# Kernel optimization log

Hardware: AMD Instinct MI355X
Metric: run time of the kernel (lower is better)

Reference implementation:

```python
import jax, jax.numpy as jnp
import numpy as np

# Stochastic-computing layer: values in [0,1] are encoded as random bitstreams
# (bit = uniform <= value), multiply = AND, and the reduction over input rows is
# a chained random MUX (tf.where with p=0.5 coins), then mean over the bit axis.
BATCH, D_IN, D_OUT, BIT_SIZE = 512, 1024, 1024, 128


def setup_inputs() -> dict:
    key = jax.random.key(0)
    kx, kw = jax.random.split(key)
    # bitstream-encoded probabilities in [0, 1]
    x = jax.random.uniform(kx, (BATCH, D_IN), dtype=jnp.float32)
    w = jax.random.uniform(kw, (D_IN, D_OUT), dtype=jnp.float32)
    return {"x": x, "w": w}


def reference(x, w):
    B, Din = x.shape
    Dout = w.shape[1]
    key = jax.random.key(42)
    kx, kw, kc = jax.random.split(key, 3)

    # bitstream generation: bit = (uniform <= value)
    x_bits = jax.random.uniform(kx, (B, Din, BIT_SIZE)) <= x[:, :, None]        # (B, Din, T) bool
    w_bits = jax.random.uniform(kw, (Din, Dout, BIT_SIZE)) <= w[:, :, None]     # (Din, Dout, T) bool

    # Chained random MUX over rows 1..Din-2 (mirrors `for row in range(1, dim-1)`):
    #   final = where(coin, final, row_r)  ->  result is row r of the LAST step
    #   whose coin was False; row 0 if every coin was True. Coins are shared
    #   across the output dim (original select_line shape (B, 1, T)).
    n_steps = Din - 2
    coins = jax.random.uniform(kc, (n_steps, B, BIT_SIZE)) <= 0.5               # (steps, B, T) bool
    rows = jnp.arange(1, Din - 1)                                               # (steps,)
    idx = jnp.max(jnp.where(~coins, rows[:, None, None], 0), axis=0)            # (B, T) int

    # Gather the selected row's bits instead of materializing (B, Din, Dout, T)
    chosen_x = jnp.take_along_axis(x_bits, idx[:, None, :], axis=1)[:, 0, :]    # (B, T)
    w_bt = jnp.transpose(w_bits, (0, 2, 1))                                     # (Din, T, Dout)
    chosen_w = w_bt[idx, jnp.arange(BIT_SIZE)[None, :], :]                      # (B, T, Dout)

    # stochastic multiply (AND) then decode via mean over the bit axis
    final = (chosen_x[:, :, None] & chosen_w).astype(jnp.float32)               # (B, T, Dout)
    return jnp.mean(final, axis=1)                                              # (B, Dout)
```

## Files before the change

kernel.cpp:

```cpp
#include <hip/hip_runtime.h>
#include <stdint.h>

#define BATCH 512
#define D_IN 1024
#define D_OUT 1024
#define BITSZ 128
#define N_STEPS (D_IN - 2)

#define IBASE 960
#define ICAP 64

#define WS_V_OFF 0u
#define WS_V_BYTES (BATCH * BITSZ * 4u)
#define WS_TAB_OFF (WS_V_OFF + WS_V_BYTES)
#define WS_TAB_BYTES (BITSZ * ICAP * 32u * 4u)
#define WS_NEEDED (WS_TAB_OFF + WS_TAB_BYTES)

#define TSTRIDE 132

__host__ __device__ __forceinline__ uint32_t rotl32(uint32_t x, uint32_t d) {
  return (x << d) | (x >> (32u - d));
}

__host__ __device__ __forceinline__ void threefry2x32(uint32_t k0, uint32_t k1,
                                                      uint32_t& x0, uint32_t& x1) {
  const uint32_t k2 = k0 ^ k1 ^ 0x1BD11BDAu;
  x0 += k0; x1 += k1;
#define TFR(r) { x0 += x1; x1 = rotl32(x1, (r)); x1 ^= x0; }
  TFR(13) TFR(15) TFR(26) TFR(6)
  x0 += k1; x1 += k2 + 1u;
  TFR(17) TFR(29) TFR(16) TFR(24)
  x0 += k2; x1 += k0 + 2u;
  TFR(13) TFR(15) TFR(26) TFR(6)
  x0 += k0; x1 += k1 + 3u;
  TFR(17) TFR(29) TFR(16) TFR(24)
  x0 += k1; x1 += k2 + 4u;
  TFR(13) TFR(15) TFR(26) TFR(6)
  x0 += k2; x1 += k0 + 5u;
#undef TFR
}

__device__ __forceinline__ float runif(uint32_t k0, uint32_t k1, uint32_t n) {
  uint32_t x0 = 0u, x1 = n;
  threefry2x32(k0, k1, x0, x1);
  const uint32_t b = x0 ^ x1;
  return __uint_as_float((b >> 9) | 0x3f800000u) - 1.0f;
}

__device__ __forceinline__ int scan_idx(int b, int t,
                                        uint32_t ck0, uint32_t ck1) {
  const uint32_t bt = ((uint32_t)b << 7) + (uint32_t)t;
  int idx = 0;
  int s;
  for (s = N_STEPS - 1; s >= 3; s -= 4) {
    const float u0 = runif(ck0, ck1, ((uint32_t)(s)     << 16) + bt);
    const float u1 = runif(ck0, ck1, ((uint32_t)(s - 1) << 16) + bt);
    const float u2 = runif(ck0, ck1, ((uint32_t)(s - 2) << 16) + bt);
    const float u3 = runif(ck0, ck1, ((uint32_t)(s - 3) << 16) + bt);
    if (u0 > 0.5f) { idx = s + 1; break; }
    if (u1 > 0.5f) { idx = s;     break; }
    if (u2 > 0.5f) { idx = s - 1; break; }
    if (u3 > 0.5f) { idx = s - 2; break; }
  }
  if (idx == 0 && s < 3) {
    const float u0 = runif(ck0, ck1, (1u << 16) + bt);
    const float u1 = runif(ck0, ck1, bt);
    if (u0 > 0.5f)      idx = 2;
    else if (u1 > 0.5f) idx = 1;
  }
  return idx;
}

__global__ void __launch_bounds__(256) k_tabx(const float* __restrict__ x,
                                              const float* __restrict__ w,
                                              int* __restrict__ v,
                                              uint32_t* __restrict__ tab,
                                              uint32_t ck0, uint32_t ck1,
                                              uint32_t xk0, uint32_t xk1,
                                              uint32_t wk0, uint32_t wk1) {
  const int t = blockIdx.x & 127;
  const int q = blockIdx.x >> 7;
  const int tid = threadIdx.x;

  __shared__ uint32_t s_bm[2];
  if (tid < 2) s_bm[tid] = 0u;
  __syncthreads();

#pragma unroll
  for (int h = 0; h < 2; ++h) {
    const int b = tid + h * 256;
    const int idx = scan_idx(b, t, ck0, ck1);
    const float ux = runif(xk0, xk1,
        ((uint32_t)b << 17) + ((uint32_t)idx << 7) + (uint32_t)t);
    const int xb = (ux <= x[b * D_IN + idx]) ? 1 : 0;
    if (q == 0) v[b * BITSZ + t] = xb ? idx : -1;
    if (xb && idx >= IBASE) {
      const int bp = idx - IBASE;
      atomicOr(&s_bm[bp >> 5], 1u << (bp & 31));
    }
  }
  __syncthreads();

  unsigned long long bm = (unsigned long long)s_bm[0] |
                          ((unsigned long long)s_bm[1] << 32);
  const int d = q * 256 + tid;
  const int lane = tid & 63;
  const int wbase = (d >> 5) & ~1;
  const float* wcol = w + d;
  while (bm) {
    const int j = __builtin_ctzll(bm);
    bm &= bm - 1ull;
    const int i = IBASE + j;
    const float u = runif(wk0, wk1,
        ((uint32_t)i << 17) + ((uint32_t)d << 7) + (uint32_t)t);
    const unsigned long long mb = __ballot(u <= wcol[i * D_OUT]);
    uint32_t* row = tab + (((t << 6) + j) << 5);
    if (lane == 0)  row[wbase]     = (uint32_t)mb;
    if (lane == 32) row[wbase + 1] = (uint32_t)(mb >> 32);
  }
}

__global__ void __launch_bounds__(256) k_idx(const float* __restrict__ x,
                                             int* __restrict__ v,
                                             uint32_t ck0, uint32_t ck1,
                                             uint32_t xk0, uint32_t xk1) {
  const int tid = blockIdx.x * 256 + threadIdx.x;
  const int b = tid >> 7;
  const int t = tid & 127;
  const int idx = scan_idx(b, t, ck0, ck1);
  const float ux = runif(xk0, xk1,
      ((uint32_t)b << 17) + ((uint32_t)idx << 7) + (uint32_t)t);
  const int xb = (ux <= x[b * D_IN + idx]) ? 1 : 0;
  v[tid] = xb ? idx : -1;
}

__global__ void __launch_bounds__(1024) k_acc(const float* __restrict__ w,
                                              const int* __restrict__ v,
                                              const uint32_t* __restrict__ tab,
                                              float* __restrict__ out,
                                              uint32_t wk0, uint32_t wk1,
                                              int use_tab) {
  const int b = blockIdx.x;
  const int tid = threadIdx.x;

  __shared__ __align__(16) uint32_t s_tab2[32 * TSTRIDE];
  __shared__ int s_list[BITSZ];
  __shared__ int s_wcnt[2];
  __shared__ int s_anyfb;

  if (tid == 0) s_anyfb = use_tab ? 0 : 1;

  unsigned long long mb = 0;
  int code = -1;
  bool act = false;
  if (tid < BITSZ) {
    code = v[b * BITSZ + tid];
    act = code >= 0;
    mb = __ballot(act);
    if ((tid & 63) == 0) s_wcnt[tid >> 6] = __popcll(mb);
  }
  __syncthreads();
  const int m = s_wcnt[0] + s_wcnt[1];
  const int m4 = (m + 3) & ~3;
  if (tid < BITSZ && act) {
    const int lane = tid & 63;
    const int pos = ((tid >= 64) ? s_wcnt[0] : 0) +
                    __popcll(mb & ((1ull << lane) - 1ull));
    s_list[pos] = (code << 7) | tid;
    if (code < IBASE) atomicOr(&s_anyfb, 1);
  }
  __syncthreads();

  if (s_anyfb == 0) {
    const int wrd = tid & 31;
    for (int jj = tid >> 5; jj < m; jj += 32) {
      const int e = s_list[jj];
      const int i = e >> 7, t = e & 127;
      s_tab2[wrd * TSTRIDE + jj] = tab[(((t << 6) + (i - IBASE)) << 5) + wrd];
    }
    if (tid < 32)
      for (int jj = m; jj < m4; ++jj) s_tab2[tid * TSTRIDE + jj] = 0u;
    __syncthreads();

    const int dw = tid >> 5, db = tid & 31;
    const uint32_t* colp = &s_tab2[dw * TSTRIDE];
    int acc = 0;
    for (int k = 0; k < m4; k += 4) {
      const uint4 r = *(const uint4*)(colp + k);
      acc += (r.x >> db) & 1u;
      acc += (r.y >> db) & 1u;
      acc += (r.z >> db) & 1u;
      acc += (r.w >> db) & 1u;
    }
    out[b * D_OUT + tid] = (float)acc * (1.0f / (float)BITSZ);
  } else {
    int acc = 0;
    for (int jj = 0; jj < m; ++jj) {
      const int e = s_list[jj];
      const int i = e >> 7, t = e & 127;
      const float u = runif(wk0, wk1,
          ((uint32_t)i << 17) + ((uint32_t)tid << 7) + (uint32_t)t);
      acc += (u <= w[i * D_OUT + tid]) ? 1 : 0;
    }
    out[b * D_OUT + tid] = (float)acc * (1.0f / (float)BITSZ);
  }
}

struct TFKeys { uint32_t xk0, xk1, wk0, wk1, ck0, ck1; };

static TFKeys derive_keys() {
  TFKeys K;
  uint32_t a0 = 0, a1 = 0; threefry2x32(0u, 42u, a0, a1); K.xk0 = a0; K.xk1 = a1;
  uint32_t b0 = 0, b1 = 1; threefry2x32(0u, 42u, b0, b1); K.wk0 = b0; K.wk1 = b1;
  uint32_t c0 = 0, c1 = 2; threefry2x32(0u, 42u, c0, c1); K.ck0 = c0; K.ck1 = c1;
  return K;
}

extern "C" void kernel_launch(void* const* d_in, const int* in_sizes, int n_in,
                              void* d_out, int out_size, void* d_ws, size_t ws_size,
                              hipStream_t stream) {
  const float* x = (const float*)d_in[0];
  const float* w = (const float*)d_in[1];
  if (n_in >= 2 && in_sizes[0] == D_IN * D_OUT && in_sizes[1] == BATCH * D_IN) {
    const float* tmp = x; x = w; w = tmp;
  }
  float* out = (float*)d_out;
  char* ws = (char*)d_ws;
  int* v = (int*)(ws + WS_V_OFF);
  uint32_t* tab = (uint32_t*)(ws + WS_TAB_OFF);

  const int use_tab = (ws_size >= WS_NEEDED) ? 1 : 0;
  const TFKeys K = derive_keys();

  if (use_tab) {
    hipLaunchKernelGGL(k_tabx, dim3(BITSZ * 4), dim3(256), 0, stream,
                       x, w, v, tab, K.ck0, K.ck1, K.xk0, K.xk1, K.wk0, K.wk1);
  } else {
    hipLaunchKernelGGL(k_idx, dim3((BATCH * BITSZ) / 256), dim3(256), 0, stream,
                       x, v, K.ck0, K.ck1, K.xk0, K.xk1);
  }
  hipLaunchKernelGGL(k_acc, dim3(BATCH), dim3(D_OUT), 0, stream,
                     w, v, tab, out, K.wk0, K.wk1, use_tab);
}
```

Before: 25.14 us.

## Split index scan from table build and halve k_acc block size

In the before code, k_tabx recomputed the expensive coin scan four times per (b,t), once for each of its four output-column groups. The change runs the scan once per (b,t) in k_idx, which also writes a transposed copy vt. A new k_tab kernel then builds the bitmask of needed rows from vt with a wave OR-reduction and fills the w-bit table using 1024-thread blocks. k_acc now uses 512 threads that each produce two outputs. This removes the redundant scan work but adds a third kernel launch and an extra global round trip through vt.

```diff
diff --git a/kernel.cpp b/kernel.cpp
--- a/kernel.cpp
+++ b/kernel.cpp
@@ -12,7 +12,9 @@
 
 #define WS_V_OFF 0u
 #define WS_V_BYTES (BATCH * BITSZ * 4u)
-#define WS_TAB_OFF (WS_V_OFF + WS_V_BYTES)
+#define WS_VT_OFF (WS_V_OFF + WS_V_BYTES)
+#define WS_VT_BYTES (BITSZ * BATCH * 4u)
+#define WS_TAB_OFF (WS_VT_OFF + WS_VT_BYTES)
 #define WS_TAB_BYTES (BITSZ * ICAP * 32u * 4u)
 #define WS_NEEDED (WS_TAB_OFF + WS_TAB_BYTES)
 
@@ -47,9 +49,7 @@
   return __uint_as_float((b >> 9) | 0x3f800000u) - 1.0f;
 }
 
-__device__ __forceinline__ int scan_idx(int b, int t,
-                                        uint32_t ck0, uint32_t ck1) {
-  const uint32_t bt = ((uint32_t)b << 7) + (uint32_t)t;
+__device__ __forceinline__ int scan_idx(uint32_t bt, uint32_t ck0, uint32_t ck1) {
   int idx = 0;
   int s;
   for (s = N_STEPS - 1; s >= 3; s -= 4) {
@@ -71,45 +71,64 @@
   return idx;
 }
 
-__global__ void __launch_bounds__(256) k_tabx(const float* __restrict__ x,
-                                              const float* __restrict__ w,
-                                              int* __restrict__ v,
+__global__ void __launch_bounds__(256) k_idx(const float* __restrict__ x,
+                                             int* __restrict__ v,
+                                             int* __restrict__ vt,
+                                             uint32_t ck0, uint32_t ck1,
+                                             uint32_t xk0, uint32_t xk1,
+                                             int use_tab) {
+  const int tid = blockIdx.x * 256 + threadIdx.x;
+  const int b = tid >> 7;
+  const int t = tid & 127;
+  const int idx = scan_idx((uint32_t)tid, ck0, ck1);
+  const float ux = runif(xk0, xk1,
+      ((uint32_t)b << 17) + ((uint32_t)idx << 7) + (uint32_t)t);
+  const int xb = (ux <= x[b * D_IN + idx]) ? 1 : 0;
+  const int val = xb ? idx : -1;
+  v[tid] = val;
+  if (use_tab) vt[t * BATCH + b] = val;
+}
+
+__global__ void __launch_bounds__(1024) k_tab(const float* __restrict__ w,
+                                              const int* __restrict__ vt,
                                               uint32_t* __restrict__ tab,
-                                              uint32_t ck0, uint32_t ck1,
-                                              uint32_t xk0, uint32_t xk1,
                                               uint32_t wk0, uint32_t wk1) {
-  const int t = blockIdx.x & 127;
-  const int q = blockIdx.x >> 7;
+  const int t = blockIdx.x >> 1;
+  const int h = blockIdx.x & 1;
   const int tid = threadIdx.x;
 
   __shared__ uint32_t s_bm[2];
+  __shared__ int s_rows[ICAP];
   if (tid < 2) s_bm[tid] = 0u;
   __syncthreads();
 
-#pragma unroll
-  for (int h = 0; h < 2; ++h) {
-    const int b = tid + h * 256;
-    const int idx = scan_idx(b, t, ck0, ck1);
-    const float ux = runif(xk0, xk1,
-        ((uint32_t)b << 17) + ((uint32_t)idx << 7) + (uint32_t)t);
-    const int xb = (ux <= x[b * D_IN + idx]) ? 1 : 0;
-    if (q == 0) v[b * BITSZ + t] = xb ? idx : -1;
-    if (xb && idx >= IBASE) {
-      const int bp = idx - IBASE;
-      atomicOr(&s_bm[bp >> 5], 1u << (bp & 31));
-    }
-  }
-  __syncthreads();
-
-  unsigned long long bm = (unsigned long long)s_bm[0] |
-                          ((unsigned long long)s_bm[1] << 32);
-  const int d = q * 256 + tid;
+  unsigned long long m64 = 0;
+  if (tid < BATCH) {
+    const int code = vt[t * BATCH + tid];
+    if (code >= IBASE) m64 = 1ull << (code - IBASE);
+  }
+  for (int off = 32; off; off >>= 1) m64 |= __shfl_down(m64, off);
+  if ((tid & 63) == 0 && tid < BATCH) {
+    if ((uint32_t)m64)         atomicOr(&s_bm[0], (uint32_t)m64);
+    if ((uint32_t)(m64 >> 32)) atomicOr(&s_bm[1], (uint32_t)(m64 >> 32));
+  }
+  __syncthreads();
+
+  const unsigned long long bm = (unsigned long long)s_bm[0] |
+                                ((unsigned long long)s_bm[1] << 32);
+  const int cnt = __popcll(bm);
+  if (tid < 64 && ((bm >> tid) & 1ull))
+    s_rows[__popcll(bm & ((1ull << tid) - 1ull))] = tid;
+  __syncthreads();
+
+  const int g = (tid < 512) ? 0 : 1;
+  const int dl = (tid < 512) ? tid : (tid - 512);
+  const int d = h * 512 + dl;
   const int lane = tid & 63;
   const int wbase = (d >> 5) & ~1;
   const float* wcol = w + d;
-  while (bm) {
-    const int j = __builtin_ctzll(bm);
-    bm &= bm - 1ull;
+  for (int r = g; r < cnt; r += 2) {
+    const int j = s_rows[r];
     const int i = IBASE + j;
     const float u = runif(wk0, wk1,
         ((uint32_t)i << 17) + ((uint32_t)d << 7) + (uint32_t)t);
@@ -120,26 +139,12 @@
   }
 }
 
-__global__ void __launch_bounds__(256) k_idx(const float* __restrict__ x,
-                                             int* __restrict__ v,
-                                             uint32_t ck0, uint32_t ck1,
-                                             uint32_t xk0, uint32_t xk1) {
-  const int tid = blockIdx.x * 256 + threadIdx.x;
-  const int b = tid >> 7;
-  const int t = tid & 127;
-  const int idx = scan_idx(b, t, ck0, ck1);
-  const float ux = runif(xk0, xk1,
-      ((uint32_t)b << 17) + ((uint32_t)idx << 7) + (uint32_t)t);
-  const int xb = (ux <= x[b * D_IN + idx]) ? 1 : 0;
-  v[tid] = xb ? idx : -1;
-}
-
-__global__ void __launch_bounds__(1024) k_acc(const float* __restrict__ w,
-                                              const int* __restrict__ v,
-                                              const uint32_t* __restrict__ tab,
-                                              float* __restrict__ out,
-                                              uint32_t wk0, uint32_t wk1,
-                                              int use_tab) {
+__global__ void __launch_bounds__(512) k_acc(const float* __restrict__ w,
+                                             const int* __restrict__ v,
+                                             const uint32_t* __restrict__ tab,
+                                             float* __restrict__ out,
+                                             uint32_t wk0, uint32_t wk1,
+                                             int use_tab) {
   const int b = blockIdx.x;
   const int tid = threadIdx.x;
 
@@ -173,7 +178,7 @@
 
   if (s_anyfb == 0) {
     const int wrd = tid & 31;
-    for (int jj = tid >> 5; jj < m; jj += 32) {
+    for (int jj = tid >> 5; jj < m; jj += 16) {
       const int e = s_list[jj];
       const int i = e >> 7, t = e & 127;
       s_tab2[wrd * TSTRIDE + jj] = tab[(((t << 6) + (i - IBASE)) << 5) + wrd];
@@ -182,27 +187,36 @@
       for (int jj = m; jj < m4; ++jj) s_tab2[tid * TSTRIDE + jj] = 0u;
     __syncthreads();
 
-    const int dw = tid >> 5, db = tid & 31;
-    const uint32_t* colp = &s_tab2[dw * TSTRIDE];
-    int acc = 0;
+    const int dw0 = tid >> 5, db = tid & 31;
+    const int dw1 = dw0 + 16;
+    const uint32_t* c0 = &s_tab2[dw0 * TSTRIDE];
+    const uint32_t* c1 = &s_tab2[dw1 * TSTRIDE];
+    int a0 = 0, a1 = 0;
     for (int k = 0; k < m4; k += 4) {
-      const uint4 r = *(const uint4*)(colp + k);
-      acc += (r.x >> db) & 1u;
-      acc += (r.y >> db) & 1u;
-      acc += (r.z >> db) & 1u;
-      acc += (r.w >> db) & 1u;
+      const uint4 r0 = *(const uint4*)(c0 + k);
+      const uint4 r1 = *(const uint4*)(c1 + k);
+      a0 += (r0.x >> db) & 1u; a0 += (r0.y >> db) & 1u;
+      a0 += (r0.z >> db) & 1u; a0 += (r0.w >> db) & 1u;
+      a1 += (r1.x >> db) & 1u; a1 += (r1.y >> db) & 1u;
+      a1 += (r1.z >> db) & 1u; a1 += (r1.w >> db) & 1u;
     }
-    out[b * D_OUT + tid] = (float)acc * (1.0f / (float)BITSZ);
+    out[b * D_OUT + tid]       = (float)a0 * (1.0f / (float)BITSZ);
+    out[b * D_OUT + tid + 512] = (float)a1 * (1.0f / (float)BITSZ);
   } else {
-    int acc = 0;
+    const int d0 = tid, d1 = tid + 512;
+    int a0 = 0, a1 = 0;
     for (int jj = 0; jj < m; ++jj) {
       const int e = s_list[jj];
       const int i = e >> 7, t = e & 127;
-      const float u = runif(wk0, wk1,
-          ((uint32_t)i << 17) + ((uint32_t)tid << 7) + (uint32_t)t);
-      acc += (u <= w[i * D_OUT + tid]) ? 1 : 0;
+      const float u0 = runif(wk0, wk1,
+          ((uint32_t)i << 17) + ((uint32_t)d0 << 7) + (uint32_t)t);
+      const float u1 = runif(wk0, wk1,
+          ((uint32_t)i << 17) + ((uint32_t)d1 << 7) + (uint32_t)t);
+      a0 += (u0 <= w[i * D_OUT + d0]) ? 1 : 0;
+      a1 += (u1 <= w[i * D_OUT + d1]) ? 1 : 0;
     }
-    out[b * D_OUT + tid] = (float)acc * (1.0f / (float)BITSZ);
+    out[b * D_OUT + d0] = (float)a0 * (1.0f / (float)BITSZ);
+    out[b * D_OUT + d1] = (float)a1 * (1.0f / (float)BITSZ);
   }
 }
 
@@ -227,18 +241,17 @@
   float* out = (float*)d_out;
   char* ws = (char*)d_ws;
   int* v = (int*)(ws + WS_V_OFF);
+  int* vt = (int*)(ws + WS_VT_OFF);
   uint32_t* tab = (uint32_t*)(ws + WS_TAB_OFF);
 
   const int use_tab = (ws_size >= WS_NEEDED) ? 1 : 0;
   const TFKeys K = derive_keys();
 
-  if (use_tab) {
-    hipLaunchKernelGGL(k_tabx, dim3(BITSZ * 4), dim3(256), 0, stream,
-                       x, w, v, tab, K.ck0, K.ck1, K.xk0, K.xk1, K.wk0, K.wk1);
-  } else {
-    hipLaunchKernelGGL(k_idx, dim3((BATCH * BITSZ) / 256), dim3(256), 0, stream,
-                       x, v, K.ck0, K.ck1, K.xk0, K.xk1);
-  }
-  hipLaunchKernelGGL(k_acc, dim3(BATCH), dim3(D_OUT), 0, stream,
+  hipLaunchKernelGGL(k_idx, dim3((BATCH * BITSZ) / 256), dim3(256), 0, stream,
+                     x, v, vt, K.ck0, K.ck1, K.xk0, K.xk1, use_tab);
+  if (use_tab)
+    hipLaunchKernelGGL(k_tab, dim3(BITSZ * 2), dim3(1024), 0, stream,
+                       w, vt, tab, K.wk0, K.wk1);
+  hipLaunchKernelGGL(k_acc, dim3(BATCH), dim3(512), 0, stream,
                      w, v, tab, out, K.wk0, K.wk1, use_tab);
 }
```

After: 22.39 us. 1.12x faster.
